# Kernel optimization log

Hardware: AMD Instinct MI355X
Metric: run time of the kernel (lower is better)

## Reference

```python
import jax, jax.numpy as jnp
import numpy as np

D = 512            # d_model
H = 4              # num_heads
DK = D // 2        # total key dim (expand_k = 0.5)
DV = D             # total value dim (expand_v = 1.0)
HK = DK // H       # per-head key dim  = 64
HV = DV // H       # per-head value dim = 128
GATE_LOW_RANK = 16
GATE_LOGIT_NORMALIZER = 16.0
LN_EPS = 1e-5


def setup_inputs() -> dict:
    key = jax.random.key(0)
    ks = jax.random.split(key, 9)
    B, S = 2, 16384
    g = lambda k, shape, scale: (jax.random.normal(k, shape, dtype=jnp.float32) * scale)
    return {
        "x":    g(ks[0], (B, S, D), 1.0),
        "Wq":   g(ks[1], (D, DK), D ** -0.5),
        "Wk":   g(ks[2], (D, DK), D ** -0.5),
        "Wv":   g(ks[3], (D, DV), D ** -0.5),
        "Wg":   g(ks[4], (D, DV), D ** -0.5),
        "Wgk1": g(ks[5], (D, GATE_LOW_RANK), D ** -0.5),
        "Wgk2": g(ks[6], (GATE_LOW_RANK, DK), GATE_LOW_RANK ** -0.5),
        "bgk2": jnp.zeros((DK,), jnp.float32),
        "Wo":   g(ks[7], (DV, D), DV ** -0.5),
    }


def _gla(x, Wq, Wk, Wv, Wg, Wgk1, Wgk2, bgk2, Wo):
    B, S, _ = x.shape
    q = (x @ Wq).reshape(B, S, H, HK) * (HK ** -0.5)   # [B,S,H,HK]
    k = (x @ Wk).reshape(B, S, H, HK)
    v = (x @ Wv).reshape(B, S, H, HV)
    g = (x @ Wg).reshape(B, S, H, HV)                  # output gate
    # low-rank forget gate, in log space
    gk = jax.nn.log_sigmoid((x @ Wgk1) @ Wgk2 + bgk2) / GATE_LOGIT_NORMALIZER
    gk = gk.reshape(B, S, H, HK)

    # gated linear recurrence over time:
    #   h_t = diag(exp(gk_t)) h_{t-1} + k_t^T v_t ;  o_t = q_t h_t
    def step(h, inp):
        q_t, k_t, v_t, gk_t = inp                      # [B,H,HK] / [B,H,HV]
        h = jnp.exp(gk_t)[..., None] * h + k_t[..., None] * v_t[..., None, :]
        o_t = jnp.einsum('bhk,bhkv->bhv', q_t, h)
        return h, o_t

    h0 = jnp.zeros((B, H, HK, HV), x.dtype)
    xs = (q.swapaxes(0, 1), k.swapaxes(0, 1), v.swapaxes(0, 1), gk.swapaxes(0, 1))
    _, o = jax.lax.scan(step, h0, xs)                  # o: [S,B,H,HV]
    o = o.swapaxes(0, 1)                               # [B,S,H,HV]

    # per-head LayerNorm (no affine) + swish output gate
    mu = o.mean(-1, keepdims=True)
    var = ((o - mu) ** 2).mean(-1, keepdims=True)
    o = (o - mu) * jax.lax.rsqrt(var + LN_EPS)
    o = o * jax.nn.silu(g)
    return o.reshape(B, S, DV) @ Wo                    # [B,S,D]


def reference(x, Wq, Wk, Wv, Wg, Wgk1, Wgk2, bgk2, Wo):
    return _gla(x, Wq, Wk, Wv, Wg, Wgk1, Wgk2, bgk2, Wo)
```

## Files before the change

### kernel.cpp

```cpp
#include <hip/hip_runtime.h>
#include <hip/hip_bf16.h>


typedef __hip_bfloat16 bf16;
typedef _Float16 f16;
typedef _Float16 half8 __attribute__((ext_vector_type(8)));
typedef float f32x4 __attribute__((ext_vector_type(4)));
typedef short short8 __attribute__((ext_vector_type(8)));

#define DEV static __device__ __forceinline__

DEV float b2f(bf16 v) { return __bfloat162float(v); }
DEV bf16 f2b(float v) { return __float2bfloat16(v); }
DEV float bits2f(unsigned int u16) {
    union { unsigned int u; float f; } c; c.u = u16 << 16; return c.f;
}
DEV short f2bs(float v) {
    union { bf16 h; short s; } u; u.h = __float2bfloat16(v); return u.s;
}
DEV unsigned short f2bu(float v) {
    union { bf16 h; unsigned short s; } u; u.h = __float2bfloat16(v); return u.s;
}
DEV short f2hs(float v) {
    union { f16 h; short s; } u; u.h = (f16)v; return u.s;
}
DEV float fast_rcp(float v) { return __builtin_amdgcn_rcpf(v); }

DEV float ldf(const float* p) { return *p; }
DEV float ldf(const bf16* p) { return b2f(*p); }
DEV void stf(float* p, float v) { *p = v; }
DEV void stf(bf16* p, float v) { *p = f2b(v); }

DEV float4 ld4(const float* p) { return *(const float4*)p; }
DEV float4 ld4(const bf16* p) {
    const uint2 r = *(const uint2*)p;
    return make_float4(bits2f(r.x & 0xffffu), bits2f(r.x >> 16),
                       bits2f(r.y & 0xffffu), bits2f(r.y >> 16));
}

DEV half8 ld8h(const float* p) {
    const float4 a = *(const float4*)p, b = *(const float4*)(p + 4);
    half8 h;
    h[0] = (f16)a.x; h[1] = (f16)a.y; h[2] = (f16)a.z; h[3] = (f16)a.w;
    h[4] = (f16)b.x; h[5] = (f16)b.y; h[6] = (f16)b.z; h[7] = (f16)b.w;
    return h;
}
DEV half8 ld8h(const f16* p) { return *(const half8*)p; }

DEV f32x4 mfma_bf(short8 a, short8 b, f32x4 c) {
    return __builtin_amdgcn_mfma_f32_16x16x32_bf16(a, b, c, 0, 0, 0);
}
DEV f32x4 mfma_h(half8 a, half8 b, f32x4 c) {
    return __builtin_amdgcn_mfma_f32_16x16x32_f16(a, b, c, 0, 0, 0);
}

DEV void gl_lds16(const f16* g, f16* l) {
    __builtin_amdgcn_global_load_lds(
        (const __attribute__((address_space(1))) void*)g,
        (__attribute__((address_space(3))) void*)l, 16, 0, 0);
}

DEV size_t voff(int v, int t) {
    return (size_t)(((((v >> 4) * 2 + (t >> 5)) * 4 + ((t >> 3) & 3)) * 16
                     + (v & 15)) * 8 + (t & 7));
}

__global__ __launch_bounds__(256) void cvt_xh_k(
    const float* __restrict__ x, f16* __restrict__ xh)
{
    const size_t i = ((size_t)blockIdx.x * 256 + threadIdx.x) * 8;
    *(half8*)&xh[i] = ld8h(&x[i]);
}

__global__ __launch_bounds__(256) void cvt_wt_k(
    const float* __restrict__ Wq, const float* __restrict__ Wk,
    const float* __restrict__ Wv, const float* __restrict__ Wg,
    const float* __restrict__ Wo, f16* __restrict__ Wt)
{
    __shared__ float tile[64][65];
    const int nb = blockIdx.x * 64;
    const int tid = threadIdx.x;
    const float* src; int nloc, N;
    if (nb < 256)       { src = Wq; N = 256; nloc = nb; }
    else if (nb < 512)  { src = Wk; N = 256; nloc = nb - 256; }
    else if (nb < 1024) { src = Wv; N = 512; nloc = nb - 512; }
    else if (nb < 1536) { src = Wg; N = 512; nloc = nb - 1024; }
    else                { src = Wo; N = 512; nloc = nb - 1536; }
    for (int k0 = 0; k0 < 512; k0 += 64) {
        for (int e = tid; e < 4096; e += 256) {
            const int i = e >> 6, j = e & 63;
            tile[i][j] = src[(size_t)(k0 + i) * N + nloc + j];
        }
        __syncthreads();
        for (int e = tid; e < 4096; e += 256) {
            const int j = e >> 6, i = e & 63;
            Wt[(size_t)(nb + j) * 512 + k0 + i] = (f16)tile[i][j];
        }
        __syncthreads();
    }
}

__global__ __launch_bounds__(256) void proj_gemm_k(
    const f16* __restrict__ A, const f16* __restrict__ Wt,
    bf16* __restrict__ Qb, bf16* __restrict__ Kb,
    bf16* __restrict__ VF, bf16* __restrict__ GOb)
{
    __shared__ __align__(16) f16 As[128][64];
    __shared__ __align__(16) f16 Bs[128][64];
    const int bm = blockIdx.x * 128;
    const int bn = blockIdx.y * 128;
    const int tid = threadIdx.x;
    const int lane = tid & 63;
    const int wid = tid >> 6;
    const int wr = wid >> 1, wc = wid & 1;
    const int al = lane & 15;
    const int kg = lane >> 4;
    const int al7 = al & 7;

    f32x4 acc[4][4];
#pragma unroll
    for (int m = 0; m < 4; ++m)
#pragma unroll
        for (int n = 0; n < 4; ++n)
#pragma unroll
            for (int r = 0; r < 4; ++r) acc[m][n][r] = 0.f;

    const int srow = wid * 32 + (lane >> 3);
    const int sswz = ((lane & 7) ^ (lane >> 3)) << 3;
    const f16* ap = A + (size_t)(bm + srow) * 512 + sswz;
    const f16* bp = Wt + (size_t)(bn + srow) * 512 + sswz;

    for (int k0 = 0; k0 < 512; k0 += 64) {
        if (k0) __syncthreads();
#pragma unroll
        for (int i = 0; i < 4; ++i) {
            gl_lds16(ap + (size_t)i * 8 * 512 + k0, &As[wid * 32 + i * 8][0]);
            gl_lds16(bp + (size_t)i * 8 * 512 + k0, &Bs[wid * 32 + i * 8][0]);
        }
        __syncthreads();
#pragma unroll
        for (int ks = 0; ks < 2; ++ks) {
            half8 af[4], bfr[4];
            const int sp = ((ks * 4 + kg) ^ al7) << 3;
#pragma unroll
            for (int m = 0; m < 4; ++m)
                af[m] = *(const half8*)&As[wr * 64 + m * 16 + al][sp];
#pragma unroll
            for (int n = 0; n < 4; ++n)
                bfr[n] = *(const half8*)&Bs[wc * 64 + n * 16 + al][sp];
#pragma unroll
            for (int m = 0; m < 4; ++m)
#pragma unroll
                for (int n = 0; n < 4; ++n)
                    acc[m][n] = mfma_h(af[m], bfr[n], acc[m][n]);
        }
    }

    const int r00 = bm + wr * 64 + kg * 4;
    const int c00 = bn + wc * 64 + al;
    const int seg = bn >> 8;
    if (seg == 0) {
#pragma unroll
        for (int m = 0; m < 4; ++m)
#pragma unroll
            for (int n = 0; n < 4; ++n)
#pragma unroll
                for (int r = 0; r < 4; ++r)
                    stf(&Qb[(size_t)(r00 + m * 16 + r) * 256 + c00 + n * 16],
                        acc[m][n][r] * 0.125f);
    } else if (seg == 1) {
#pragma unroll
        for (int m = 0; m < 4; ++m)
#pragma unroll
            for (int n = 0; n < 4; ++n)
#pragma unroll
                for (int r = 0; r < 4; ++r)
                    stf(&Kb[(size_t)(r00 + m * 16 + r) * 256 + (c00 - 256) + n * 16],
                        acc[m][n][r]);
    } else if (seg <= 3) {
#pragma unroll
        for (int m = 0; m < 4; ++m) {
            const int row0 = r00 + m * 16;
            const int bi = row0 >> 14;
            const int chunk = (row0 >> 6) & 255;
            const int tc = row0 & 63;
#pragma unroll
            for (int n = 0; n < 4; ++n) {
                const int col = c00 - 512 + n * 16;
                const int h = col >> 7, v = col & 127;
                bf16* dst = VF + (size_t)((bi * 4 + h) * 256 + chunk) * 8192
                               + voff(v, tc);
                ushort4 pk;
                pk.x = f2bu(acc[m][n][0]); pk.y = f2bu(acc[m][n][1]);
                pk.z = f2bu(acc[m][n][2]); pk.w = f2bu(acc[m][n][3]);
                *(ushort4*)dst = pk;
            }
        }
    } else {
#pragma unroll
        for (int m = 0; m < 4; ++m)
#pragma unroll
            for (int n = 0; n < 4; ++n)
#pragma unroll
                for (int r = 0; r < 4; ++r) {
                    const float v = acc[m][n][r];
                    const float sil = v * fast_rcp(1.f + __expf(-v));
                    stf(&GOb[(size_t)(r00 + m * 16 + r) * 512 + (c00 - 1024) + n * 16],
                        sil);
                }
    }
}

__global__ __launch_bounds__(256) void gemm_bt_k(
    const f16* __restrict__ A, const f16* __restrict__ Bt,
    float* __restrict__ C)
{
    __shared__ __align__(16) f16 As[128][64];
    __shared__ __align__(16) f16 Bs[128][64];
    const int bm = blockIdx.x * 128;
    const int bn = blockIdx.y * 128;
    const int tid = threadIdx.x;
    const int lane = tid & 63;
    const int wid = tid >> 6;
    const int wr = wid >> 1, wc = wid & 1;
    const int al = lane & 15;
    const int kg = lane >> 4;
    const int al7 = al & 7;

    f32x4 acc[4][4];
#pragma unroll
    for (int m = 0; m < 4; ++m)
#pragma unroll
        for (int n = 0; n < 4; ++n)
#pragma unroll
            for (int r = 0; r < 4; ++r) acc[m][n][r] = 0.f;

    const int srow = wid * 32 + (lane >> 3);
    const int sswz = ((lane & 7) ^ (lane >> 3)) << 3;
    const f16* ap = A + (size_t)(bm + srow) * 512 + sswz;
    const f16* bp = Bt + (size_t)(bn + srow) * 512 + sswz;

    for (int k0 = 0; k0 < 512; k0 += 64) {
        if (k0) __syncthreads();
#pragma unroll
        for (int i = 0; i < 4; ++i) {
            gl_lds16(ap + (size_t)i * 8 * 512 + k0, &As[wid * 32 + i * 8][0]);
            gl_lds16(bp + (size_t)i * 8 * 512 + k0, &Bs[wid * 32 + i * 8][0]);
        }
        __syncthreads();
#pragma unroll
        for (int ks = 0; ks < 2; ++ks) {
            half8 af[4], bfr[4];
            const int sp = ((ks * 4 + kg) ^ al7) << 3;
#pragma unroll
            for (int m = 0; m < 4; ++m)
                af[m] = *(const half8*)&As[wr * 64 + m * 16 + al][sp];
#pragma unroll
            for (int n = 0; n < 4; ++n)
                bfr[n] = *(const half8*)&Bs[wc * 64 + n * 16 + al][sp];
#pragma unroll
            for (int m = 0; m < 4; ++m)
#pragma unroll
                for (int n = 0; n < 4; ++n)
                    acc[m][n] = mfma_h(af[m], bfr[n], acc[m][n]);
        }
    }
    const int r0 = bm + wr * 64 + kg * 4;
    const int c0 = bn + wc * 64 + al;
#pragma unroll
    for (int m = 0; m < 4; ++m)
#pragma unroll
        for (int n = 0; n < 4; ++n)
#pragma unroll
            for (int r = 0; r < 4; ++r)
                C[(size_t)(r0 + m * 16 + r) * 512 + c0 + n * 16] = acc[m][n][r];
}

__global__ __launch_bounds__(256) void gate_mfma_k(
    const f16* __restrict__ xh, const float* __restrict__ Wgk1,
    const float* __restrict__ Wgk2, const float* __restrict__ bgk2,
    bf16* __restrict__ GK)
{
    __shared__ __align__(16) f16 As[128][40];
    __shared__ __align__(16) f16 w1s[16][520];
    __shared__ float tls[128][17];
    const int bm = blockIdx.x * 128;
    const int tid = threadIdx.x;
    const int lane = tid & 63;
    const int wid = tid >> 6;
    const int al = lane & 15;
    const int kg = lane >> 4;
    const int kg8 = kg * 8;

    for (int e = tid; e < 8192; e += 256) {
        const int kk = e >> 4, n = e & 15;
        w1s[n][kk] = (f16)Wgk1[e];
    }

    f32x4 acc[2];
#pragma unroll
    for (int m = 0; m < 2; ++m)
#pragma unroll
        for (int r = 0; r < 4; ++r) acc[m][r] = 0.f;

    const int ar = tid >> 1;
    const int ac = (tid & 1) * 16;
    for (int k0 = 0; k0 < 512; k0 += 32) {
        {
            const f16* ap = xh + (size_t)(bm + ar) * 512 + k0 + ac;
            *(half8*)&As[ar][ac] = *(const half8*)ap;
            *(half8*)&As[ar][ac + 8] = *(const half8*)(ap + 8);
        }
        __syncthreads();
        const half8 bfr = *(const half8*)&w1s[al][k0 + kg8];
#pragma unroll
        for (int m = 0; m < 2; ++m) {
            const half8 af = *(const half8*)&As[wid * 32 + m * 16 + al][kg8];
            acc[m] = mfma_h(af, bfr, acc[m]);
        }
        __syncthreads();
    }
#pragma unroll
    for (int m = 0; m < 2; ++m)
#pragma unroll
        for (int r = 0; r < 4; ++r)
            tls[wid * 32 + m * 16 + kg * 4 + r][al] = acc[m][r];
    __syncthreads();

    float w2[16];
#pragma unroll
    for (int r = 0; r < 16; ++r) w2[r] = Wgk2[r * 256 + tid];
    const float bb = bgk2[tid];
    bf16* gout = GK + (size_t)bm * 256 + tid;
    for (int m = 0; m < 128; ++m) {
        float z = bb;
#pragma unroll
        for (int r = 0; r < 16; ++r) z = fmaf(tls[m][r], w2[r], z);
        const float ls = fminf(z, 0.f) - __logf(1.f + __expf(-fabsf(z)));
        stf(&gout[(size_t)m * 256], ls * (1.f / 16.f));
    }
}

__global__ __launch_bounds__(256) void chunk_state_k(
    const bf16* __restrict__ Km, const bf16* __restrict__ VF,
    const bf16* __restrict__ GKm, bf16* __restrict__ CS,
    float* __restrict__ DD)
{
    __shared__ __align__(16) short k2t[64][72];
    __shared__ float cpart[4][64];
    const int blk = blockIdx.x;
    const int chunk = blk & 255;
    const int bh = blk >> 8;
    const int bi = bh >> 2, h = bh & 3;
    const int rowbase = bi * 16384 + chunk * 64;
    const int tid = threadIdx.x;
    const int k = tid & 63, tg = tid >> 6;

    float g[16];
    {
        float run = 0.f;
#pragma unroll
        for (int j = 0; j < 16; ++j) {
            run += ldf(&GKm[(size_t)(rowbase + tg * 16 + j) * 256 + h * 64 + k]);
            g[j] = run;
        }
        cpart[tg][k] = run;
    }
    __syncthreads();
    float off = 0.f;
#pragma unroll
    for (int s = 0; s < 3; ++s) if (s < tg) off += cpart[s][k];
    const float tot = cpart[0][k] + cpart[1][k] + cpart[2][k] + cpart[3][k];
    if (tg == 0) DD[(size_t)blk * 64 + k] = __expf(tot);

    {
        short8 p0, p1;
#pragma unroll
        for (int j = 0; j < 16; ++j) {
            const float kv = ldf(&Km[(size_t)(rowbase + tg * 16 + j) * 256 + h * 64 + k]);
            const float w = kv * __expf(tot - (g[j] + off));
            if (j < 8) p0[j] = f2bs(w); else p1[j - 8] = f2bs(w);
        }
        *(short8*)&k2t[k][tg * 16] = p0;
        *(short8*)&k2t[k][tg * 16 + 8] = p1;
    }
    __syncthreads();

    const int lane = tid & 63, wid = tid >> 6;
    const int al = lane & 15, kg = lane >> 4, kg8 = kg * 8;
    const bf16* Vtb = VF + (size_t)blk * 8192;

    short8 xf[2][2];
#pragma unroll
    for (int m = 0; m < 2; ++m)
#pragma unroll
        for (int ks = 0; ks < 2; ++ks)
            xf[m][ks] = *(const short8*)&Vtb[(size_t)(((wid * 2 + m) * 2 + ks) * 64 + lane) * 8];
    short8 yf[2][4];
#pragma unroll
    for (int ks = 0; ks < 2; ++ks)
#pragma unroll
        for (int n = 0; n < 4; ++n)
            yf[ks][n] = *(const short8*)&k2t[n * 16 + al][ks * 32 + kg8];

    f32x4 acc[2][4];
#pragma unroll
    for (int m = 0; m < 2; ++m)
#pragma unroll
        for (int n = 0; n < 4; ++n)
#pragma unroll
            for (int r = 0; r < 4; ++r) acc[m][n][r] = 0.f;
#pragma unroll
    for (int ks = 0; ks < 2; ++ks)
#pragma unroll
        for (int m = 0; m < 2; ++m)
#pragma unroll
            for (int n = 0; n < 4; ++n)
                acc[m][n] = mfma_bf(xf[m][ks], yf[ks][n], acc[m][n]);

    bf16* out = CS + (size_t)blk * 8192;
#pragma unroll
    for (int m = 0; m < 2; ++m)
#pragma unroll
        for (int n = 0; n < 4; ++n)
#pragma unroll
            for (int r = 0; r < 4; ++r)
                stf(&out[(size_t)(wid * 32 + m * 16 + kg * 4 + r) * 64 + n * 16 + al],
                    acc[m][n][r]);
}

__global__ __launch_bounds__(256) void scan_k(
    const bf16* __restrict__ CS, const float* __restrict__ DD,
    bf16* __restrict__ HF)
{
    const int bh = blockIdx.x >> 5;
    const int slice = blockIdx.x & 31;
    const int tid = threadIdx.x;
    const int e = slice * 256 + tid;
    const int v = e >> 6, k = e & 63;
    float H = 0.f;
    const bf16* base = CS + (size_t)bh * 256 * 8192 + e;
    bf16* hbase = HF + (size_t)bh * 256 * 8192 + voff(v, k);
    const float* dbase = DD + (size_t)bh * 256 * 64 + k;
#pragma unroll 4
    for (int n = 0; n < 256; ++n) {
        const float s = ldf(&base[(size_t)n * 8192]);
        const float d = dbase[(size_t)n * 64];
        stf(&hbase[(size_t)n * 8192], H);
        H = fmaf(d, H, s);
    }
}

__global__ __launch_bounds__(256) void chunk_out_k(
    const bf16* __restrict__ Qm, const bf16* __restrict__ Km,
    const bf16* __restrict__ VF, const bf16* __restrict__ GKm,
    const bf16* __restrict__ HF, bf16* GO)
{
    __shared__ __align__(16) short qs[64][72];
    __shared__ __align__(16) short ks[64][72];
    __shared__ __align__(16) short ab[64][72];
    __shared__ float cpart[4][64];

    const int blk = blockIdx.x;
    const int chunk = blk & 255;
    const int bh = blk >> 8;
    const int bi = bh >> 2, h = bh & 3;
    const int rowbase = bi * 16384 + chunk * 64;
    const int tid = threadIdx.x;
    const int k = tid & 63, tg = tid >> 6;

    float g[16];
    {
        float run = 0.f;
#pragma unroll
        for (int j = 0; j < 16; ++j) {
            run += ldf(&GKm[(size_t)(rowbase + tg * 16 + j) * 256 + h * 64 + k]);
            g[j] = run;
        }
        cpart[tg][k] = run;
    }
    __syncthreads();
    float off = 0.f;
#pragma unroll
    for (int s = 0; s < 3; ++s) if (s < tg) off += cpart[s][k];

#pragma unroll
    for (int j = 0; j < 16; ++j) {
        const int t = tg * 16 + j;
        const size_t idx = (size_t)(rowbase + t) * 256 + h * 64 + k;
        const float gc = g[j] + off;
        const float eg = __expf(gc);
        qs[t][k] = f2bs(ldf(&Qm[idx]) * eg);
        ks[t][k] = f2bs(ldf(&Km[idx]) * fast_rcp(eg));
    }
    __syncthreads();

    const int lane = tid & 63, wid = tid >> 6;
    const int al = lane & 15, kg = lane >> 4;
    const int w16 = wid * 16, kg8 = kg * 8;

    short8 xq[2];
    xq[0] = *(const short8*)&qs[w16 + al][kg8];
    xq[1] = *(const short8*)&qs[w16 + al][32 + kg8];

    f32x4 aacc[4];
#pragma unroll
    for (int n = 0; n < 4; ++n)
#pragma unroll
        for (int r = 0; r < 4; ++r) aacc[n][r] = 0.f;
#pragma unroll
    for (int ksb = 0; ksb < 2; ++ksb)
#pragma unroll
        for (int n = 0; n < 4; ++n) {
            const short8 y = *(const short8*)&ks[n * 16 + al][ksb * 32 + kg8];
            aacc[n] = mfma_bf(xq[ksb], y, aacc[n]);
        }
#pragma unroll
    for (int n = 0; n < 4; ++n)
#pragma unroll
        for (int r = 0; r < 4; ++r) {
            const int tt = w16 + kg * 4 + r;
            const int ii = n * 16 + al;
            ab[tt][ii] = (ii <= tt) ? f2bs(aacc[n][r]) : (short)0;
        }
    short8 xa[2];
    xa[0] = *(const short8*)&ab[w16 + al][kg8];
    xa[1] = *(const short8*)&ab[w16 + al][32 + kg8];

    const bf16* Vtb = VF + (size_t)blk * 8192;
    const bf16* Hb = HF + (size_t)blk * 8192;
    f32x4 oacc[8];
#pragma unroll
    for (int n = 0; n < 8; ++n)
#pragma unroll
        for (int r = 0; r < 4; ++r) oacc[n][r] = 0.f;
#pragma unroll
    for (int n = 0; n < 8; ++n) {
        const size_t f0 = (size_t)((n * 2 + 0) * 64 + lane) * 8;
        const size_t f1 = (size_t)((n * 2 + 1) * 64 + lane) * 8;
        const short8 yv0 = *(const short8*)&Vtb[f0];
        const short8 yv1 = *(const short8*)&Vtb[f1];
        const short8 yh0 = *(const short8*)&Hb[f0];
        const short8 yh1 = *(const short8*)&Hb[f1];
        oacc[n] = mfma_bf(xa[0], yv0, oacc[n]);
        oacc[n] = mfma_bf(xa[1], yv1, oacc[n]);
        oacc[n] = mfma_bf(xq[0], yh0, oacc[n]);
        oacc[n] = mfma_bf(xq[1], yh1, oacc[n]);
    }

    float psum[4] = {0.f, 0.f, 0.f, 0.f}, psq[4] = {0.f, 0.f, 0.f, 0.f};
#pragma unroll
    for (int n = 0; n < 8; ++n)
#pragma unroll
        for (int r = 0; r < 4; ++r) {
            const float v = oacc[n][r];
            psum[r] += v; psq[r] = fmaf(v, v, psq[r]);
        }
#pragma unroll
    for (int offx = 1; offx < 16; offx <<= 1)
#pragma unroll
        for (int r = 0; r < 4; ++r) {
            psum[r] += __shfl_xor(psum[r], offx);
            psq[r] += __shfl_xor(psq[r], offx);
        }
#pragma unroll
    for (int r = 0; r < 4; ++r) {
        const float mu = psum[r] * (1.f / 128.f);
        const float var = psq[r] * (1.f / 128.f) - mu * mu;
        const float rstd = rsqrtf(fmaxf(var, 0.f) + 1e-5f);
        const int row = rowbase + w16 + kg * 4 + r;
        short* gop = (short*)(GO + (size_t)row * 512 + h * 128 + al);
#pragma unroll
        for (int n = 0; n < 8; ++n) {
            const bf16 gb = *(const bf16*)&gop[n * 16];
            const float sil = b2f(gb);
            gop[n * 16] = f2hs((oacc[n][r] - mu) * rstd * sil);
        }
    }
}

__global__ __launch_bounds__(256) void zero_k(float* out, int n) {
    const int i = blockIdx.x * 256 + threadIdx.x;
    if (i < n) out[i] = 0.f;
}

static void run_all(const float* x, const float* Wq, const float* Wk,
                    const float* Wv, const float* Wg, const float* Wgk1,
                    const float* Wgk2, const float* bgk2, const float* Wo,
                    float* out, char* ws, hipStream_t stream)
{
    const int M = 32768;
    auto aln = [](size_t v) { return (v + 255) & ~(size_t)255; };
    char* cur = ws;
    bf16* Qb = (bf16*)cur;  cur += aln((size_t)M * 256 * 2);
    bf16* Kb = (bf16*)cur;  cur += aln((size_t)M * 256 * 2);
    bf16* Vfb = (bf16*)cur; cur += aln((size_t)M * 512 * 2);
    bf16* GOb = (bf16*)cur; cur += aln((size_t)M * 512 * 2);
    bf16* Hfb = (bf16*)cur; cur += aln((size_t)2048 * 8192 * 2);
    float* DDb = (float*)cur; cur += aln((size_t)2048 * 64 * 4);
    f16* Wtb = (f16*)cur;   cur += aln((size_t)2048 * 512 * 2);
    bf16* GKb = (bf16*)cur; cur += aln((size_t)M * 256 * 2);
    bf16* CSb = (bf16*)cur;
    f16* xh = (f16*)CSb;

    const dim3 blk(256);
    cvt_xh_k<<<dim3(8192), blk, 0, stream>>>(x, xh);
    cvt_wt_k<<<dim3(32), blk, 0, stream>>>(Wq, Wk, Wv, Wg, Wo, Wtb);
    proj_gemm_k<<<dim3(M / 128, 12), blk, 0, stream>>>(xh, Wtb, Qb, Kb, Vfb, GOb);
    gate_mfma_k<<<dim3(M / 128), blk, 0, stream>>>(xh, Wgk1, Wgk2, bgk2, GKb);
    chunk_state_k<<<dim3(2048), blk, 0, stream>>>(Kb, Vfb, GKb, CSb, DDb);
    scan_k<<<dim3(256), blk, 0, stream>>>(CSb, DDb, Hfb);
    chunk_out_k<<<dim3(2048), blk, 0, stream>>>(Qb, Kb, Vfb, GKb, Hfb, GOb);
    gemm_bt_k<<<dim3(M / 128, 4), blk, 0, stream>>>((const f16*)GOb,
                                                    Wtb + (size_t)1536 * 512, out);
}

extern "C" void kernel_launch(void* const* d_in, const int* in_sizes, int n_in,
                              void* d_out, int out_size, void* d_ws, size_t ws_size,
                              hipStream_t stream)
{
    const float* x    = (const float*)d_in[0];
    const float* Wq   = (const float*)d_in[1];
    const float* Wk   = (const float*)d_in[2];
    const float* Wv   = (const float*)d_in[3];
    const float* Wg   = (const float*)d_in[4];
    const float* Wgk1 = (const float*)d_in[5];
    const float* Wgk2 = (const float*)d_in[6];
    const float* bgk2 = (const float*)d_in[7];
    const float* Wo   = (const float*)d_in[8];
    float* out = (float*)d_out;

    const size_t M = 32768;
    const size_t slack = 8192;
    const size_t need = 2 * M * 256 * 2 + 2 * M * 512 * 2
                      + (size_t)2048 * 8192 * 2 + 2048 * 64 * 4
                      + (size_t)2048 * 512 * 2 + M * 256 * 2
                      + (size_t)2048 * 8192 * 2 + slack;

    if (ws_size >= need) {
        run_all(x, Wq, Wk, Wv, Wg, Wgk1, Wgk2, bgk2, Wo,
                out, (char*)d_ws, stream);
    } else {
        zero_k<<<dim3((out_size + 255) / 256), dim3(256), 0, stream>>>(out, out_size);
    }
}
```

Before: 358.5 us.

## Pre-swizzle weights into MFMA fragment order and load B directly to registers

The weight conversion kernel now writes weights in a fragment-major layout so each lane can load its MFMA B operand with one contiguous 16-byte global load. Both GEMM kernels drop the B shared-memory tile and the LDS reads for it, fetching B fragments straight from global (L2-resident) memory. This halves LDS traffic and staging per k-step, but adds global-load latency that is not hidden by the existing barrier structure and increases register use.

```diff
diff --git a/kernel.cpp b/kernel.cpp
--- a/kernel.cpp
+++ b/kernel.cpp
@@ -75,7 +75,7 @@
 __global__ __launch_bounds__(256) void cvt_wt_k(
     const float* __restrict__ Wq, const float* __restrict__ Wk,
     const float* __restrict__ Wv, const float* __restrict__ Wg,
-    const float* __restrict__ Wo, f16* __restrict__ Wt)
+    const float* __restrict__ Wo, f16* __restrict__ Wf)
 {
     __shared__ float tile[64][65];
     const int nb = blockIdx.x * 64;
@@ -92,23 +92,33 @@
             tile[i][j] = src[(size_t)(k0 + i) * N + nloc + j];
         }
         __syncthreads();
-        for (int e = tid; e < 4096; e += 256) {
-            const int j = e >> 6, i = e & 63;
-            Wt[(size_t)(nb + j) * 512 + k0 + i] = (f16)tile[i][j];
+        const int kstep = k0 >> 6;
+        for (int ow = tid; ow < 512; ow += 256) {
+            const int j = ow >> 3;
+            const int i8 = ow & 7;
+            const int n = nb + j;
+            const int pan = n >> 7, nblk = (n >> 4) & 7, al = n & 15;
+            half8 hv;
+#pragma unroll
+            for (int e = 0; e < 8; ++e) hv[e] = (f16)tile[i8 * 8 + e][j];
+            const size_t flat =
+                ((size_t)(((pan * 8 + kstep) * 2 + (i8 >> 2)) * 8 + nblk)) * 512
+                + (size_t)(((i8 & 3) * 16 + al)) * 8;
+            *(half8*)&Wf[flat] = hv;
         }
         __syncthreads();
     }
 }
 
 __global__ __launch_bounds__(256) void proj_gemm_k(
-    const f16* __restrict__ A, const f16* __restrict__ Wt,
+    const f16* __restrict__ A, const f16* __restrict__ Wf,
     bf16* __restrict__ Qb, bf16* __restrict__ Kb,
     bf16* __restrict__ VF, bf16* __restrict__ GOb)
 {
     __shared__ __align__(16) f16 As[128][64];
-    __shared__ __align__(16) f16 Bs[128][64];
     const int bm = blockIdx.x * 128;
     const int bn = blockIdx.y * 128;
+    const int pan = bn >> 7;
     const int tid = threadIdx.x;
     const int lane = tid & 63;
     const int wid = tid >> 6;
@@ -128,31 +138,34 @@
     const int srow = wid * 32 + (lane >> 3);
     const int sswz = ((lane & 7) ^ (lane >> 3)) << 3;
     const f16* ap = A + (size_t)(bm + srow) * 512 + sswz;
-    const f16* bp = Wt + (size_t)(bn + srow) * 512 + sswz;
+    const f16* wfb = Wf + (size_t)lane * 8;
 
     for (int k0 = 0; k0 < 512; k0 += 64) {
         if (k0) __syncthreads();
 #pragma unroll
-        for (int i = 0; i < 4; ++i) {
+        for (int i = 0; i < 4; ++i)
             gl_lds16(ap + (size_t)i * 8 * 512 + k0, &As[wid * 32 + i * 8][0]);
-            gl_lds16(bp + (size_t)i * 8 * 512 + k0, &Bs[wid * 32 + i * 8][0]);
-        }
+        half8 bfr[2][4];
+        const int kstep = k0 >> 6;
+#pragma unroll
+        for (int ks = 0; ks < 2; ++ks)
+#pragma unroll
+            for (int n = 0; n < 4; ++n)
+                bfr[ks][n] = *(const half8*)&wfb[
+                    (size_t)(((pan * 8 + kstep) * 2 + ks) * 8 + wc * 4 + n) * 512];
         __syncthreads();
 #pragma unroll
         for (int ks = 0; ks < 2; ++ks) {
-            half8 af[4], bfr[4];
+            half8 af[4];
             const int sp = ((ks * 4 + kg) ^ al7) << 3;
 #pragma unroll
             for (int m = 0; m < 4; ++m)
                 af[m] = *(const half8*)&As[wr * 64 + m * 16 + al][sp];
 #pragma unroll
-            for (int n = 0; n < 4; ++n)
-                bfr[n] = *(const half8*)&Bs[wc * 64 + n * 16 + al][sp];
-#pragma unroll
             for (int m = 0; m < 4; ++m)
 #pragma unroll
                 for (int n = 0; n < 4; ++n)
-                    acc[m][n] = mfma_h(af[m], bfr[n], acc[m][n]);
+                    acc[m][n] = mfma_h(af[m], bfr[ks][n], acc[m][n]);
         }
     }
 
@@ -212,13 +225,13 @@
 }
 
 __global__ __launch_bounds__(256) void gemm_bt_k(
-    const f16* __restrict__ A, const f16* __restrict__ Bt,
+    const f16* __restrict__ A, const f16* __restrict__ Wf,
     float* __restrict__ C)
 {
     __shared__ __align__(16) f16 As[128][64];
-    __shared__ __align__(16) f16 Bs[128][64];
     const int bm = blockIdx.x * 128;
     const int bn = blockIdx.y * 128;
+    const int pan = 12 + (bn >> 7);
     const int tid = threadIdx.x;
     const int lane = tid & 63;
     const int wid = tid >> 6;
@@ -238,31 +251,34 @@
     const int srow = wid * 32 + (lane >> 3);
     const int sswz = ((lane & 7) ^ (lane >> 3)) << 3;
     const f16* ap = A + (size_t)(bm + srow) * 512 + sswz;
-    const f16* bp = Bt + (size_t)(bn + srow) * 512 + sswz;
+    const f16* wfb = Wf + (size_t)lane * 8;
 
     for (int k0 = 0; k0 < 512; k0 += 64) {
         if (k0) __syncthreads();
 #pragma unroll
-        for (int i = 0; i < 4; ++i) {
+        for (int i = 0; i < 4; ++i)
             gl_lds16(ap + (size_t)i * 8 * 512 + k0, &As[wid * 32 + i * 8][0]);
-            gl_lds16(bp + (size_t)i * 8 * 512 + k0, &Bs[wid * 32 + i * 8][0]);
-        }
+        half8 bfr[2][4];
+        const int kstep = k0 >> 6;
+#pragma unroll
+        for (int ks = 0; ks < 2; ++ks)
+#pragma unroll
+            for (int n = 0; n < 4; ++n)
+                bfr[ks][n] = *(const half8*)&wfb[
+                    (size_t)(((pan * 8 + kstep) * 2 + ks) * 8 + wc * 4 + n) * 512];
         __syncthreads();
 #pragma unroll
         for (int ks = 0; ks < 2; ++ks) {
-            half8 af[4], bfr[4];
+            half8 af[4];
             const int sp = ((ks * 4 + kg) ^ al7) << 3;
 #pragma unroll
             for (int m = 0; m < 4; ++m)
                 af[m] = *(const half8*)&As[wr * 64 + m * 16 + al][sp];
 #pragma unroll
-            for (int n = 0; n < 4; ++n)
-                bfr[n] = *(const half8*)&Bs[wc * 64 + n * 16 + al][sp];
-#pragma unroll
             for (int m = 0; m < 4; ++m)
 #pragma unroll
                 for (int n = 0; n < 4; ++n)
-                    acc[m][n] = mfma_h(af[m], bfr[n], acc[m][n]);
+                    acc[m][n] = mfma_h(af[m], bfr[ks][n], acc[m][n]);
         }
     }
     const int r0 = bm + wr * 64 + kg * 4;
@@ -598,21 +614,20 @@
     bf16* GOb = (bf16*)cur; cur += aln((size_t)M * 512 * 2);
     bf16* Hfb = (bf16*)cur; cur += aln((size_t)2048 * 8192 * 2);
     float* DDb = (float*)cur; cur += aln((size_t)2048 * 64 * 4);
-    f16* Wtb = (f16*)cur;   cur += aln((size_t)2048 * 512 * 2);
+    f16* Wfb = (f16*)cur;   cur += aln((size_t)2048 * 512 * 2);
     bf16* GKb = (bf16*)cur; cur += aln((size_t)M * 256 * 2);
     bf16* CSb = (bf16*)cur;
     f16* xh = (f16*)CSb;
 
     const dim3 blk(256);
     cvt_xh_k<<<dim3(8192), blk, 0, stream>>>(x, xh);
-    cvt_wt_k<<<dim3(32), blk, 0, stream>>>(Wq, Wk, Wv, Wg, Wo, Wtb);
-    proj_gemm_k<<<dim3(M / 128, 12), blk, 0, stream>>>(xh, Wtb, Qb, Kb, Vfb, GOb);
+    cvt_wt_k<<<dim3(32), blk, 0, stream>>>(Wq, Wk, Wv, Wg, Wo, Wfb);
+    proj_gemm_k<<<dim3(M / 128, 12), blk, 0, stream>>>(xh, Wfb, Qb, Kb, Vfb, GOb);
     gate_mfma_k<<<dim3(M / 128), blk, 0, stream>>>(xh, Wgk1, Wgk2, bgk2, GKb);
     chunk_state_k<<<dim3(2048), blk, 0, stream>>>(Kb, Vfb, GKb, CSb, DDb);
     scan_k<<<dim3(256), blk, 0, stream>>>(CSb, DDb, Hfb);
     chunk_out_k<<<dim3(2048), blk, 0, stream>>>(Qb, Kb, Vfb, GKb, Hfb, GOb);
-    gemm_bt_k<<<dim3(M / 128, 4), blk, 0, stream>>>((const f16*)GOb,
-                                                    Wtb + (size_t)1536 * 512, out);
+    gemm_bt_k<<<dim3(M / 128, 4), blk, 0, stream>>>((const f16*)GOb, Wfb, out);
 }
 
 extern "C" void kernel_launch(void* const* d_in, const int* in_sizes, int n_in,
```

New measurement: 353.7 us. Within noise of the previous version (-1.3%).
